# Performance work log

Measured on AMD Instinct MI355X. Metric: run time of the kernel, lower is better.

Reference implementation:

```python
import jax, jax.numpy as jnp
import numpy as np

N = 1024   # num_points
H = 256
W = 256
T = 2      # frames
DEG = 2    # polynomial degree for xyz/cholesky
DEG_OP = 2 # opacity polynomial degree


def setup_inputs() -> dict:
    key = jax.random.key(0)
    k1, k2, k3, k4, k5, k6 = jax.random.split(key, 6)
    # xyz: c0 = atanh(2*(U-0.5)) as in torch init, higher orders small
    u = jax.random.uniform(k1, (1, N, 2), minval=1e-4, maxval=1.0 - 1e-4)
    xyz_c0 = jnp.arctanh(2.0 * u - 1.0)
    xyz_hi = jax.random.normal(k2, (DEG, N, 2)) * 0.05
    xyz_coeffs = jnp.concatenate([xyz_c0, xyz_hi], axis=0).astype(jnp.float32)
    # cholesky: c0 = [1,0,1] + 0.01*noise, higher orders small (matches torch init scale)
    chol_c0 = jnp.array([1.0, 0.0, 1.0])[None, None, :] + jax.random.normal(k3, (1, N, 3)) * 0.01
    chol_hi = jax.random.normal(k4, (DEG, N, 3)) * 0.01
    cholesky_coeffs = jnp.concatenate([chol_c0, chol_hi], axis=0).astype(jnp.float32)
    # opacity logits: start near sigmoid(2) ~ 0.88
    op_c0 = 2.0 + jax.random.normal(k5, (1, N, 1)) * 0.1
    op_hi = jax.random.normal(jax.random.fold_in(k5, 1), (DEG_OP, N, 1)) * 0.1
    opacity_coeffs = jnp.concatenate([op_c0, op_hi], axis=0).astype(jnp.float32)
    features = jax.random.normal(k6, (N, 3)).astype(jnp.float32)
    return {"xyz_coeffs": xyz_coeffs, "cholesky_coeffs": cholesky_coeffs,
            "opacity_coeffs": opacity_coeffs, "features": features}


def _t_power(num_t, deg):
    t = jnp.linspace(0.0, 1.0, num_t)
    return jnp.stack([t ** i for i in range(deg + 1)], axis=1)  # (T, deg+1)


CHOL_BOUND = jnp.array([0.5, 0.0, 0.5], dtype=jnp.float32)
PIX_SCALE = jnp.array([W, H], dtype=jnp.float32)


def _render_frame(xy, chol, opac, colors):
    # xy: (N,2) in [-1,1]; chol: (N,3) L-elements; opac: (N,); colors: (N,3)
    means = 0.5 * (xy + 1.0) * PIX_SCALE            # (N,2) pixel space
    l1, l2, l3 = chol[:, 0], chol[:, 1], chol[:, 2]
    # Sigma = L L^T with L=[[l1,0],[l2,l3]]
    s11 = l1 * l1
    s12 = l1 * l2
    s22 = l2 * l2 + l3 * l3
    det = jnp.maximum(s11 * s22 - s12 * s12, 1e-8)
    a = s22 / det   # conic xx
    b = -s12 / det  # conic xy
    c = s11 / det   # conic yy
    dx = (jnp.arange(W, dtype=jnp.float32) + 0.5)[:, None] - means[:, 0][None, :]  # (W,N)
    dy = (jnp.arange(H, dtype=jnp.float32) + 0.5)[:, None] - means[:, 1][None, :]  # (H,N)
    # sigma = 0.5*a*dx^2 + b*dx*dy + 0.5*c*dy^2, built (H,W,N) with separable pieces
    sigma = (0.5 * a * dx * dx)[None, :, :] + (0.5 * c * dy * dy)[:, None, :] \
            + b * dy[:, None, :] * dx[None, :, :]
    w = opac * jnp.exp(-sigma)                       # (H,W,N)
    img = jnp.einsum('hwn,nc->hwc', w, colors)       # accumulated-sum rasterization
    return jnp.clip(img, 0.0, 1.0)


def reference(xyz_coeffs, cholesky_coeffs, opacity_coeffs, features):
    tp = _t_power(T, DEG)          # (T, DEG+1)
    tp_op = _t_power(T, DEG_OP)    # (T, DEG_OP+1)
    xy_t = jnp.tanh(jnp.einsum('td,dnc->tnc', tp, xyz_coeffs))            # (T,N,2)
    chol_t = jnp.einsum('td,dnc->tnc', tp, cholesky_coeffs) + CHOL_BOUND  # (T,N,3)
    opac_t = jax.nn.sigmoid(jnp.einsum('td,dnc->tnc', tp_op, opacity_coeffs))[..., 0]  # (T,N)
    colors = jax.nn.sigmoid(features)                                     # (N,3)
    imgs = jax.vmap(lambda xy, ch, op: _render_frame(xy, ch, op, colors))(xy_t, chol_t, opac_t)
    return jnp.transpose(imgs, (0, 3, 1, 2))  # (T,3,H,W)
```

## Files before the change

kernel.cpp:

```cpp
#include <hip/hip_runtime.h>
#include <math.h>

#define N_G   1024
#define W_IMG 256
#define H_IMG 256
#define T_FR  2
#define CULL_E (-20.0f)

__global__ __launch_bounds__(256) void gi_render(
    const float* __restrict__ xyz,
    const float* __restrict__ chol,
    const float* __restrict__ opc,
    const float* __restrict__ feat,
    float* __restrict__ out)
{
    __shared__ float4 s_geo[N_G];
    __shared__ float4 s_col[N_G];
    __shared__ int    s_count;

    const int tid = threadIdx.x;
    const int bid = blockIdx.x;
    const int t   = bid >> 8;
    const int y   = bid & 255;
    const float py = (float)y + 0.5f;

    if (tid == 0) s_count = 0;
    __syncthreads();

    const float tt = (float)t;
    const float p1 = tt;
    const float p2 = tt * tt;
    const float L2E = 1.4426950408889634f;

    #pragma unroll
    for (int g = 0; g < N_G / 256; ++g) {
        const int n = g * 256 + tid;

        float x0 = xyz[n*2 + 0] + xyz[(N_G + n)*2 + 0]*p1 + xyz[(2*N_G + n)*2 + 0]*p2;
        float x1 = xyz[n*2 + 1] + xyz[(N_G + n)*2 + 1]*p1 + xyz[(2*N_G + n)*2 + 1]*p2;
        float mx = 0.5f * (tanhf(x0) + 1.0f) * (float)W_IMG;
        float my = 0.5f * (tanhf(x1) + 1.0f) * (float)H_IMG;

        float l1 = chol[n*3+0] + chol[(N_G+n)*3+0]*p1 + chol[(2*N_G+n)*3+0]*p2 + 0.5f;
        float l2 = chol[n*3+1] + chol[(N_G+n)*3+1]*p1 + chol[(2*N_G+n)*3+1]*p2;
        float l3 = chol[n*3+2] + chol[(N_G+n)*3+2]*p1 + chol[(2*N_G+n)*3+2]*p2 + 0.5f;

        float s11 = l1*l1;
        float s12 = l1*l2;
        float s22 = l2*l2 + l3*l3;
        float det = fmaxf(s11*s22 - s12*s12, 1e-8f);
        float inv = 1.0f / det;
        float a =  s22 * inv;
        float b = -s12 * inv;
        float c =  s11 * inv;

        float ol = opc[n] + opc[N_G + n]*p1 + opc[2*N_G + n]*p2;
        float opv = 1.0f / (1.0f + __expf(-ol));

        float A  = -0.5f * a * L2E;
        float Bc = -b * L2E;
        float C  = -0.5f * c * L2E;
        float K  = __log2f(opv);

        float dy  = py - my;
        float Bdy = Bc * dy;
        float Kdy = fmaf(C * dy, dy, K);

        float dxl = 0.5f - mx, dxr = 255.5f - mx;
        float el = fmaf(fmaf(A, dxl, Bdy), dxl, Kdy);
        float er = fmaf(fmaf(A, dxr, Bdy), dxr, Kdy);
        float emax = fmaxf(el, er);
        float dxv = -Bdy / (2.0f * A);
        if (dxv > dxl && dxv < dxr) {
            float ev = fmaf(fmaf(A, dxv, Bdy), dxv, Kdy);
            emax = fmaxf(emax, ev);
        }

        if (emax > CULL_E) {
            int idx = atomicAdd(&s_count, 1);
            s_geo[idx] = make_float4(mx, A, Bdy, Kdy);
            float cr = 1.0f / (1.0f + __expf(-feat[n*3+0]));
            float cg = 1.0f / (1.0f + __expf(-feat[n*3+1]));
            float cb = 1.0f / (1.0f + __expf(-feat[n*3+2]));
            s_col[idx] = make_float4(cr, cg, cb, 0.0f);
        }
    }
    __syncthreads();

    const int cnt = s_count;
    const float px = (float)tid + 0.5f;
    float accr = 0.0f, accg = 0.0f, accb = 0.0f;

    for (int i = 0; i < cnt; ++i) {
        float4 gp = s_geo[i];
        float4 gc = s_col[i];
        float dx = px - gp.x;
        float e  = fmaf(gp.y, dx*dx, fmaf(gp.z, dx, gp.w));
        float w  = __builtin_amdgcn_exp2f(e);
        accr = fmaf(w, gc.x, accr);
        accg = fmaf(w, gc.y, accg);
        accb = fmaf(w, gc.z, accb);
    }

    const int base = ((t*3) << 16) + (y << 8) + tid;
    out[base            ] = fminf(fmaxf(accr, 0.0f), 1.0f);
    out[base + (1 << 16)] = fminf(fmaxf(accg, 0.0f), 1.0f);
    out[base + (2 << 16)] = fminf(fmaxf(accb, 0.0f), 1.0f);
}

extern "C" void kernel_launch(void* const* d_in, const int* in_sizes, int n_in,
                              void* d_out, int out_size, void* d_ws, size_t ws_size,
                              hipStream_t stream) {
    const float* xyz  = (const float*)d_in[0];
    const float* chol = (const float*)d_in[1];
    const float* opc  = (const float*)d_in[2];
    const float* feat = (const float*)d_in[3];
    float* out = (float*)d_out;
    gi_render<<<T_FR * H_IMG, 256, 0, stream>>>(xyz, chol, opc, feat, out);
}
```

Measured before the change: 67.95 us.

## Precompute per-Gaussian parameters in a prepass kernel and use wave-aggregated compaction

Adds a prepass kernel that computes each Gaussian's per-frame mean, conic coefficients, opacity log and colors once, writing them to workspace. Before this, all 256 row blocks recomputed them redundantly. The render kernel now loads these precomputed float4s and replaces the per-thread shared atomic with a ballot/popcount wave-level compaction. The cost is an extra kernel launch and global workspace traffic, and the order of culled Gaussians changes, which can shift float summation order slightly.

Measured after the change: 68.50 us. No clear change (+0.8%).

```diff
diff --git a/kernel.cpp b/kernel.cpp
--- a/kernel.cpp
+++ b/kernel.cpp
@@ -7,11 +7,67 @@
 #define T_FR  2
 #define CULL_E (-20.0f)
 
-__global__ __launch_bounds__(256) void gi_render(
+#define WS_P0 0
+#define WS_P1 (T_FR * N_G * 16)
+#define WS_COL (2 * T_FR * N_G * 16)
+
+__global__ __launch_bounds__(256) void gi_pre(
     const float* __restrict__ xyz,
     const float* __restrict__ chol,
     const float* __restrict__ opc,
     const float* __restrict__ feat,
+    float4* __restrict__ P0,
+    float4* __restrict__ P1,
+    float4* __restrict__ Col)
+{
+    const int i = blockIdx.x * 256 + threadIdx.x;
+    const int t = i >> 10;
+    const int n = i & (N_G - 1);
+
+    const float p1 = (float)t;
+    const float p2 = p1 * p1;
+    const float L2E = 1.4426950408889634f;
+
+    float x0 = xyz[n*2 + 0] + xyz[(N_G + n)*2 + 0]*p1 + xyz[(2*N_G + n)*2 + 0]*p2;
+    float x1 = xyz[n*2 + 1] + xyz[(N_G + n)*2 + 1]*p1 + xyz[(2*N_G + n)*2 + 1]*p2;
+    float mx = 0.5f * (tanhf(x0) + 1.0f) * (float)W_IMG;
+    float my = 0.5f * (tanhf(x1) + 1.0f) * (float)H_IMG;
+
+    float l1 = chol[n*3+0] + chol[(N_G+n)*3+0]*p1 + chol[(2*N_G+n)*3+0]*p2 + 0.5f;
+    float l2 = chol[n*3+1] + chol[(N_G+n)*3+1]*p1 + chol[(2*N_G+n)*3+1]*p2;
+    float l3 = chol[n*3+2] + chol[(N_G+n)*3+2]*p1 + chol[(2*N_G+n)*3+2]*p2 + 0.5f;
+
+    float s11 = l1*l1;
+    float s12 = l1*l2;
+    float s22 = l2*l2 + l3*l3;
+    float det = fmaxf(s11*s22 - s12*s12, 1e-8f);
+    float inv = 1.0f / det;
+    float a =  s22 * inv;
+    float b = -s12 * inv;
+    float c =  s11 * inv;
+
+    float ol = opc[n] + opc[N_G + n]*p1 + opc[2*N_G + n]*p2;
+    float opv = 1.0f / (1.0f + __expf(-ol));
+
+    float A  = -0.5f * a * L2E;
+    float Bc = -b * L2E;
+    float C  = -0.5f * c * L2E;
+    float K  = __log2f(opv);
+
+    P0[i] = make_float4(mx, my, A, Bc);
+    P1[i] = make_float4(C, K, 0.0f, 0.0f);
+    if (t == 0) {
+        float cr = 1.0f / (1.0f + __expf(-feat[n*3+0]));
+        float cg = 1.0f / (1.0f + __expf(-feat[n*3+1]));
+        float cb = 1.0f / (1.0f + __expf(-feat[n*3+2]));
+        Col[n] = make_float4(cr, cg, cb, 0.0f);
+    }
+}
+
+__global__ __launch_bounds__(256) void gi_render(
+    const float4* __restrict__ P0,
+    const float4* __restrict__ P1,
+    const float4* __restrict__ Col,
     float* __restrict__ out)
 {
     __shared__ float4 s_geo[N_G];
@@ -23,48 +79,23 @@
     const int t   = bid >> 8;
     const int y   = bid & 255;
     const float py = (float)y + 0.5f;
+    const int lane = tid & 63;
 
     if (tid == 0) s_count = 0;
     __syncthreads();
 
-    const float tt = (float)t;
-    const float p1 = tt;
-    const float p2 = tt * tt;
-    const float L2E = 1.4426950408889634f;
-
     #pragma unroll
     for (int g = 0; g < N_G / 256; ++g) {
-        const int n = g * 256 + tid;
+        const int n  = g * 256 + tid;
+        const int tn = (t << 10) + n;
+        float4 p0 = P0[tn];
+        float4 p1 = P1[tn];
 
-        float x0 = xyz[n*2 + 0] + xyz[(N_G + n)*2 + 0]*p1 + xyz[(2*N_G + n)*2 + 0]*p2;
-        float x1 = xyz[n*2 + 1] + xyz[(N_G + n)*2 + 1]*p1 + xyz[(2*N_G + n)*2 + 1]*p2;
-        float mx = 0.5f * (tanhf(x0) + 1.0f) * (float)W_IMG;
-        float my = 0.5f * (tanhf(x1) + 1.0f) * (float)H_IMG;
-
-        float l1 = chol[n*3+0] + chol[(N_G+n)*3+0]*p1 + chol[(2*N_G+n)*3+0]*p2 + 0.5f;
-        float l2 = chol[n*3+1] + chol[(N_G+n)*3+1]*p1 + chol[(2*N_G+n)*3+1]*p2;
-        float l3 = chol[n*3+2] + chol[(N_G+n)*3+2]*p1 + chol[(2*N_G+n)*3+2]*p2 + 0.5f;
-
-        float s11 = l1*l1;
-        float s12 = l1*l2;
-        float s22 = l2*l2 + l3*l3;
-        float det = fmaxf(s11*s22 - s12*s12, 1e-8f);
-        float inv = 1.0f / det;
-        float a =  s22 * inv;
-        float b = -s12 * inv;
-        float c =  s11 * inv;
-
-        float ol = opc[n] + opc[N_G + n]*p1 + opc[2*N_G + n]*p2;
-        float opv = 1.0f / (1.0f + __expf(-ol));
-
-        float A  = -0.5f * a * L2E;
-        float Bc = -b * L2E;
-        float C  = -0.5f * c * L2E;
-        float K  = __log2f(opv);
-
-        float dy  = py - my;
-        float Bdy = Bc * dy;
-        float Kdy = fmaf(C * dy, dy, K);
+        float mx  = p0.x;
+        float A   = p0.z;
+        float dy  = py - p0.y;
+        float Bdy = p0.w * dy;
+        float Kdy = fmaf(p1.x * dy, dy, p1.y);
 
         float dxl = 0.5f - mx, dxr = 255.5f - mx;
         float el = fmaf(fmaf(A, dxl, Bdy), dxl, Kdy);
@@ -72,17 +103,18 @@
         float emax = fmaxf(el, er);
         float dxv = -Bdy / (2.0f * A);
         if (dxv > dxl && dxv < dxr) {
-            float ev = fmaf(fmaf(A, dxv, Bdy), dxv, Kdy);
-            emax = fmaxf(emax, ev);
+            emax = fmaxf(emax, fmaf(fmaf(A, dxv, Bdy), dxv, Kdy));
         }
 
-        if (emax > CULL_E) {
-            int idx = atomicAdd(&s_count, 1);
+        bool keep = emax > CULL_E;
+        unsigned long long m = __ballot(keep);
+        int base;
+        if (lane == 0) base = atomicAdd(&s_count, __popcll(m));
+        base = __shfl(base, 0);
+        if (keep) {
+            int idx = base + __popcll(m & ((1ull << lane) - 1ull));
             s_geo[idx] = make_float4(mx, A, Bdy, Kdy);
-            float cr = 1.0f / (1.0f + __expf(-feat[n*3+0]));
-            float cg = 1.0f / (1.0f + __expf(-feat[n*3+1]));
-            float cb = 1.0f / (1.0f + __expf(-feat[n*3+2]));
-            s_col[idx] = make_float4(cr, cg, cb, 0.0f);
+            s_col[idx] = Col[n];
         }
     }
     __syncthreads();
@@ -116,5 +148,12 @@
     const float* opc  = (const float*)d_in[2];
     const float* feat = (const float*)d_in[3];
     float* out = (float*)d_out;
-    gi_render<<<T_FR * H_IMG, 256, 0, stream>>>(xyz, chol, opc, feat, out);
+
+    char* ws = (char*)d_ws;
+    float4* P0  = (float4*)(ws + WS_P0);
+    float4* P1  = (float4*)(ws + WS_P1);
+    float4* Col = (float4*)(ws + WS_COL);
+
+    gi_pre<<<(T_FR * N_G) / 256, 256, 0, stream>>>(xyz, chol, opc, feat, P0, P1, Col);
+    gi_render<<<T_FR * H_IMG, 256, 0, stream>>>(P0, P1, Col, out);
 }
```
